# Kernel optimization log

Measured on AMD Instinct MI355X. Metric: run time of the kernel, lower is better.

The kernel has to match this reference:

```python
import jax, jax.numpy as jnp
import numpy as np

MARGIN1 = 0.05
MARGIN2 = 0.09
CAPTION_COUNT = 21
GAMMA = 1.0
P = 0.02
REG = -1.0 / 5.0          # reg passed to ot.sinkhorn (negative, as in the source)
N_ITER = 50               # numItermax=50
B = 8192
N = CAPTION_COUNT + B     # 8213


def _sinkhorn(M):
    """POT ot.sinkhorn (sinkhorn_knopp) with uniform marginals, fixed N_ITER iters.
    K = exp(-M/reg); v = b/(K^T u); u = a/(K v); T = diag(u) K diag(v)."""
    n_a, n_b = M.shape
    K = jnp.exp(-M / REG)                       # note REG < 0 -> exp(5*M)
    a = jnp.full((n_a,), 1.0 / n_a, M.dtype)
    b = jnp.full((n_b,), 1.0 / n_b, M.dtype)
    u0 = jnp.full((n_a,), 1.0 / n_a, M.dtype)
    v0 = jnp.full((n_b,), 1.0 / n_b, M.dtype)

    def body(i, uv):
        u, v = uv
        v = b / (K.T @ u)
        u = a / (K @ v)
        return (u, v)

    u, v = jax.lax.fori_loop(0, N_ITER, body, (u0, v0))
    return u[:, None] * K * v[None, :]


def setup_inputs() -> dict:
    key = jax.random.key(0)
    k1, k2 = jax.random.split(key)
    dist = jax.random.normal(k1, (B, N), dtype=jnp.float32)
    labels = jax.random.randint(k2, (B, N), 0, 4, dtype=jnp.int32)
    return {"dist": dist, "labels": labels}


def reference(dist, labels):
    relu = jax.nn.relu
    # ---- part 1: OT partial-order loss over full dist matrix ----
    scores = dist - dist[:, :1]                                   # subtract column 0
    gm0 = relu(-P - scores) + relu(scores)
    gm1 = relu(MARGIN1 + scores)
    gm2 = relu(-MARGIN2 - scores)
    gm3 = relu(MARGIN2 + scores)
    m0 = (labels == 0).astype(dist.dtype)
    m12 = ((labels == 1) | (labels == 2)).astype(dist.dtype)
    m3 = (labels == 3).astype(dist.dtype)
    GM = m0 * gm0 + m12 * (gm1 + gm2) + m3 * gm3
    expGM = jnp.exp(-GAMMA * GM)
    T = jax.lax.stop_gradient(_sinkhorn(expGM))                   # detached in torch
    T = T / T.sum(axis=1, keepdims=True)
    loss1 = jnp.mean(GM * T)

    # ---- part 2: hinge OT loss on square block dist[:, caption_count:] ----
    s = dist[:, CAPTION_COUNT:]                                   # [B, B]
    s = s - jnp.diagonal(s)[None, :]                              # subtract diag as row
    eye = jnp.eye(s.shape[0], dtype=s.dtype)
    hinge = relu(MARGIN2 + s)
    pos = relu(-0.5 - s)
    GM2 = eye * pos + (1.0 - eye) * hinge
    GM2 = jnp.where(eye > 0.5, 0.0, GM2)                          # masked_fill diag
    expGM2 = jnp.exp(-GAMMA * GM2)
    scores2 = eye * pos + (1.0 - eye) * hinge                     # redefined scores
    T2 = jax.lax.stop_gradient(_sinkhorn(expGM2))
    T2 = jnp.where(eye > 0.5, 0.0, T2)                            # zero diag
    T2 = T2 / T2.sum(axis=1, keepdims=True)
    loss2 = jnp.mean(scores2 * T2)

    return loss1 + loss2
```

## Files before the change

### kernel.cpp

```cpp
#include <hip/hip_runtime.h>

#define R     8192
#define C1    8213
#define C2    8192
#define KROW  8224
#define TROW  8192
#define NKC   514
#define NTC   512
#define CPF   8224

typedef float f32x2 __attribute__((ext_vector_type(2)));

__device__ __forceinline__ void fp8x16_to_f(const int4 w, float f[16]) {
    f32x2 p;
    p = __builtin_amdgcn_cvt_pk_f32_fp8(w.x, false); f[0]  = p.x; f[1]  = p.y;
    p = __builtin_amdgcn_cvt_pk_f32_fp8(w.x, true);  f[2]  = p.x; f[3]  = p.y;
    p = __builtin_amdgcn_cvt_pk_f32_fp8(w.y, false); f[4]  = p.x; f[5]  = p.y;
    p = __builtin_amdgcn_cvt_pk_f32_fp8(w.y, true);  f[6]  = p.x; f[7]  = p.y;
    p = __builtin_amdgcn_cvt_pk_f32_fp8(w.z, false); f[8]  = p.x; f[9]  = p.y;
    p = __builtin_amdgcn_cvt_pk_f32_fp8(w.z, true);  f[10] = p.x; f[11] = p.y;
    p = __builtin_amdgcn_cvt_pk_f32_fp8(w.w, false); f[12] = p.x; f[13] = p.y;
    p = __builtin_amdgcn_cvt_pk_f32_fp8(w.w, true);  f[14] = p.x; f[15] = p.y;
}

__device__ __forceinline__ float fp8_to_f(int byte) {
    f32x2 p = __builtin_amdgcn_cvt_pk_f32_fp8(byte & 0xff, false);
    return p.x;
}

__device__ __forceinline__ float gm_label(float sc, int lab) {
    if (lab == 0) return fmaxf(-0.02f - sc, 0.0f) + fmaxf(sc, 0.0f);
    if (lab == 3) return fmaxf(0.09f + sc, 0.0f);
    return fmaxf(0.05f + sc, 0.0f) + fmaxf(-0.09f - sc, 0.0f);
}

__device__ __forceinline__ float kval(float gm) {
    return __expf(5.0f * __expf(-gm));
}

__device__ __forceinline__ float dotw(const float f[16], float4 w0, float4 w1,
                                      float4 w2, float4 w3, float p) {
    p = fmaf(f[0], w0.x, p);  p = fmaf(f[1], w0.y, p);
    p = fmaf(f[2], w0.z, p);  p = fmaf(f[3], w0.w, p);
    p = fmaf(f[4], w1.x, p);  p = fmaf(f[5], w1.y, p);
    p = fmaf(f[6], w1.z, p);  p = fmaf(f[7], w1.w, p);
    p = fmaf(f[8], w2.x, p);  p = fmaf(f[9], w2.y, p);
    p = fmaf(f[10], w2.z, p); p = fmaf(f[11], w2.w, p);
    p = fmaf(f[12], w3.x, p); p = fmaf(f[13], w3.y, p);
    p = fmaf(f[14], w3.z, p); p = fmaf(f[15], w3.w, p);
    return p;
}


__global__ __launch_bounds__(256) void build_k1(const float* __restrict__ dist,
                                                const int* __restrict__ lab,
                                                unsigned char* __restrict__ K,
                                                unsigned char* __restrict__ gm) {
    int row = blockIdx.y;
    int j0 = (blockIdx.x * 256 + threadIdx.x) * 4;
    if (j0 >= KROW) return;
    size_t ib = (size_t)row * C1;
    float d0 = dist[ib];
    float val[4], gv[4];
#pragma unroll
    for (int k = 0; k < 4; ++k) {
        int j = j0 + k;
        val[k] = 0.0f; gv[k] = 0.0f;
        if (j < C1) {
            float g = gm_label(dist[ib + j] - d0, lab[ib + j]);
            gv[k] = g;
            val[k] = kval(g);
        }
    }
    int p = 0;
    p = __builtin_amdgcn_cvt_pk_fp8_f32(val[0], val[1], p, false);
    p = __builtin_amdgcn_cvt_pk_fp8_f32(val[2], val[3], p, true);
    *reinterpret_cast<int*>(K + (size_t)row * KROW + j0) = p;
    if (gm) {
        int q = 0;
        q = __builtin_amdgcn_cvt_pk_fp8_f32(gv[0], gv[1], q, false);
        q = __builtin_amdgcn_cvt_pk_fp8_f32(gv[2], gv[3], q, true);
        *reinterpret_cast<int*>(gm + (size_t)row * KROW + j0) = q;
    }
}

__global__ __launch_bounds__(256) void diag_k(const float* __restrict__ dist,
                                              float* __restrict__ dcol) {
    int j = blockIdx.x * 256 + threadIdx.x;
    if (j < R) dcol[j] = dist[(size_t)j * C1 + 21 + j];
}

__global__ __launch_bounds__(256) void build_k2(const float* __restrict__ dist,
                                                const float* __restrict__ dcol,
                                                unsigned char* __restrict__ K,
                                                unsigned char* __restrict__ gm) {
    int row = blockIdx.y;
    int j0 = (blockIdx.x * 256 + threadIdx.x) * 4;
    if (j0 >= KROW) return;
    size_t ib = (size_t)row * C1 + 21;
    float val[4], gv[4];
#pragma unroll
    for (int k = 0; k < 4; ++k) {
        int j = j0 + k;
        val[k] = 0.0f; gv[k] = 0.0f;
        if (j < C2) {
            float s = dist[ib + j] - dcol[j];
            float g = (j == row) ? 0.0f : fmaxf(0.09f + s, 0.0f);
            gv[k] = g;
            val[k] = kval(g);
        }
    }
    int p = 0;
    p = __builtin_amdgcn_cvt_pk_fp8_f32(val[0], val[1], p, false);
    p = __builtin_amdgcn_cvt_pk_fp8_f32(val[2], val[3], p, true);
    *reinterpret_cast<int*>(K + (size_t)row * KROW + j0) = p;
    if (gm) {
        int q = 0;
        q = __builtin_amdgcn_cvt_pk_fp8_f32(gv[0], gv[1], q, false);
        q = __builtin_amdgcn_cvt_pk_fp8_f32(gv[2], gv[3], q, true);
        *reinterpret_cast<int*>(gm + (size_t)row * KROW + j0) = q;
    }
}

__global__ __launch_bounds__(256) void transpose_k(const unsigned char* __restrict__ K,
                                                   unsigned char* __restrict__ KT) {
    __shared__ unsigned char tile[64][64];
    int i0 = blockIdx.x * 64;
    int j0 = blockIdx.y * 64;
    int t = threadIdx.x;
    int r = t >> 2, cb = (t & 3) << 4;
    if (j0 + cb < KROW) {
        int4 w = *reinterpret_cast<const int4*>(K + (size_t)(i0 + r) * KROW + j0 + cb);
        *reinterpret_cast<int4*>(&tile[r][cb]) = w;
    }
    __syncthreads();
    int jl = t >> 2, ib = (t & 3) << 4;
    if (j0 + jl < KROW) {
        unsigned char tmp[16];
#pragma unroll
        for (int k = 0; k < 16; ++k) tmp[k] = tile[ib + k][jl];
        *reinterpret_cast<int4*>(KT + (size_t)(j0 + jl) * TROW + i0 + ib) =
            *reinterpret_cast<const int4*>(tmp);
    }
}

__global__ __launch_bounds__(256) void fill_f(float* __restrict__ p, int n, float val) {
    int i = blockIdx.x * 256 + threadIdx.x;
    if (i < n) p[i] = val;
}

__global__ __launch_bounds__(256) void v_pass(const unsigned char* __restrict__ KT,
                                              const float* __restrict__ u,
                                              float* __restrict__ v,
                                              int C, float bval) {
    __shared__ float4 wp[4][516];
    int tx = threadIdx.x;
    {
        const float4* g = reinterpret_cast<const float4*>(u);
        float4 a = g[tx];
        float4 b = g[tx + 256];
        wp[tx & 3][tx >> 2] = a;
        wp[tx & 3][(tx >> 2) + 64] = b;
        float4 c2 = g[tx + 512];
        float4 d2 = g[tx + 768];
        wp[tx & 3][(tx >> 2) + 128] = c2;
        wp[tx & 3][(tx >> 2) + 192] = d2;
        float4 e2 = g[tx + 1024];
        float4 f2 = g[tx + 1280];
        wp[tx & 3][(tx >> 2) + 256] = e2;
        wp[tx & 3][(tx >> 2) + 320] = f2;
        float4 g2 = g[tx + 1536];
        float4 h2 = g[tx + 1792];
        wp[tx & 3][(tx >> 2) + 384] = g2;
        wp[tx & 3][(tx >> 2) + 448] = h2;
    }
    __syncthreads();
    int lane = tx & 63, wv = tx >> 6;
    const int4* KTb = reinterpret_cast<const int4*>(KT);
    int ra = blockIdx.x * 8 + wv * 2;
    const int4* K0 = KTb + (size_t)ra * NTC;
    const int4* K1 = K0 + NTC;
    float p0 = 0.0f, p1 = 0.0f;
#pragma unroll
    for (int s = 0; s < 8; ++s) {
        int ch = s * 64 + lane;
        float4 w0 = wp[0][ch], w1 = wp[1][ch], w2 = wp[2][ch], w3 = wp[3][ch];
        float f[16];
        fp8x16_to_f(K0[ch], f);
        p0 = dotw(f, w0, w1, w2, w3, p0);
        fp8x16_to_f(K1[ch], f);
        p1 = dotw(f, w0, w1, w2, w3, p1);
    }
#pragma unroll
    for (int off = 32; off; off >>= 1) {
        p0 += __shfl_down(p0, off, 64);
        p1 += __shfl_down(p1, off, 64);
    }
    if (lane == 0) {
        v[ra]     = (ra < C)     ? bval / p0 : 0.0f;
        v[ra + 1] = (ra + 1 < C) ? bval / p1 : 0.0f;
    }
}

__global__ __launch_bounds__(256) void u_pass(const unsigned char* __restrict__ K,
                                              const float* __restrict__ v,
                                              float* __restrict__ u, float aval) {
    __shared__ float4 wp[4][516];
    int tx = threadIdx.x;
    {
        const float4* g = reinterpret_cast<const float4*>(v);
#pragma unroll
        for (int k = 0; k < 8; ++k) {
            float4 a = g[tx + k * 256];
            wp[tx & 3][(tx >> 2) + k * 64] = a;
        }
        if (tx < 8) {
            float4 a = g[2048 + tx];
            wp[tx & 3][(tx >> 2) + 512] = a;
        }
    }
    __syncthreads();
    int lane = tx & 63, wv = tx >> 6;
    const int4* Kb = reinterpret_cast<const int4*>(K);
    int ra = blockIdx.x * 8 + wv * 2;
    const int4* K0 = Kb + (size_t)ra * NKC;
    const int4* K1 = K0 + NKC;
    float p0 = 0.0f, p1 = 0.0f;
#pragma unroll
    for (int s = 0; s < 8; ++s) {
        int ch = s * 64 + lane;
        float4 w0 = wp[0][ch], w1 = wp[1][ch], w2 = wp[2][ch], w3 = wp[3][ch];
        float f[16];
        fp8x16_to_f(K0[ch], f);
        p0 = dotw(f, w0, w1, w2, w3, p0);
        fp8x16_to_f(K1[ch], f);
        p1 = dotw(f, w0, w1, w2, w3, p1);
    }
    if (lane < 2) {
        int ch = 512 + lane;
        float4 w0 = wp[0][ch], w1 = wp[1][ch], w2 = wp[2][ch], w3 = wp[3][ch];
        float f[16];
        fp8x16_to_f(K0[ch], f);
        p0 = dotw(f, w0, w1, w2, w3, p0);
        fp8x16_to_f(K1[ch], f);
        p1 = dotw(f, w0, w1, w2, w3, p1);
    }
#pragma unroll
    for (int off = 32; off; off >>= 1) {
        p0 += __shfl_down(p0, off, 64);
        p1 += __shfl_down(p1, off, 64);
    }
    if (lane == 0) {
        u[ra]     = aval / p0;
        u[ra + 1] = aval / p1;
    }
}


__device__ __forceinline__ float2 block_reduce_2(float x, float y, float* sb) {
#pragma unroll
    for (int off = 32; off; off >>= 1) {
        x += __shfl_down(x, off, 64);
        y += __shfl_down(y, off, 64);
    }
    if ((threadIdx.x & 63) == 0) {
        int w = threadIdx.x >> 6;
        sb[w] = x; sb[4 + w] = y;
    }
    __syncthreads();
    float2 r;
    r.x = sb[0] + sb[1] + sb[2] + sb[3];
    r.y = sb[4] + sb[5] + sb[6] + sb[7];
    __syncthreads();
    return r;
}

__global__ __launch_bounds__(256) void loss1_gm(const unsigned char* __restrict__ K,
                                                const unsigned char* __restrict__ GM,
                                                const float* __restrict__ v,
                                                float* __restrict__ ratio) {
    __shared__ float sb[8];
    int i = blockIdx.x;
    const int4* Kr = reinterpret_cast<const int4*>(K + (size_t)i * KROW);
    const int4* Gr = reinterpret_cast<const int4*>(GM + (size_t)i * KROW);
    const float4* v4 = reinterpret_cast<const float4*>(v);
    float num = 0, den = 0;
    for (int c = threadIdx.x; c < NKC; c += 256) {
        float kf[16], gf[16];
        fp8x16_to_f(Kr[c], kf);
        fp8x16_to_f(Gr[c], gf);
#pragma unroll
        for (int q = 0; q < 4; ++q) {
            float4 w = v4[c * 4 + q];
            float k0 = kf[q * 4 + 0] * w.x, k1 = kf[q * 4 + 1] * w.y;
            float k2 = kf[q * 4 + 2] * w.z, k3 = kf[q * 4 + 3] * w.w;
            den += k0 + k1 + k2 + k3;
            num = fmaf(gf[q * 4 + 0], k0, num);
            num = fmaf(gf[q * 4 + 1], k1, num);
            num = fmaf(gf[q * 4 + 2], k2, num);
            num = fmaf(gf[q * 4 + 3], k3, num);
        }
    }
    float2 r = block_reduce_2(num, den, sb);
    if (threadIdx.x == 0) ratio[i] = r.x / r.y;
}

__global__ __launch_bounds__(256) void loss2_gm(const unsigned char* __restrict__ K,
                                                const unsigned char* __restrict__ GM,
                                                const float* __restrict__ v,
                                                float* __restrict__ ratio) {
    __shared__ float sb[8];
    int i = blockIdx.x;
    const int4* Kr = reinterpret_cast<const int4*>(K + (size_t)i * KROW);
    const int4* Gr = reinterpret_cast<const int4*>(GM + (size_t)i * KROW);
    const float4* v4 = reinterpret_cast<const float4*>(v);
    float num = 0, den = 0;
    for (int c = threadIdx.x; c < NKC; c += 256) {
        float kf[16], gf[16];
        fp8x16_to_f(Kr[c], kf);
        fp8x16_to_f(Gr[c], gf);
        int jb = c * 16;
#pragma unroll
        for (int q = 0; q < 4; ++q) {
            float4 w = v4[c * 4 + q];
            float m0 = (jb + q * 4 + 0 == i) ? 0.0f : 1.0f;
            float m1 = (jb + q * 4 + 1 == i) ? 0.0f : 1.0f;
            float m2 = (jb + q * 4 + 2 == i) ? 0.0f : 1.0f;
            float m3 = (jb + q * 4 + 3 == i) ? 0.0f : 1.0f;
            float k0 = kf[q * 4 + 0] * w.x * m0, k1 = kf[q * 4 + 1] * w.y * m1;
            float k2 = kf[q * 4 + 2] * w.z * m2, k3 = kf[q * 4 + 3] * w.w * m3;
            den += k0 + k1 + k2 + k3;
            num = fmaf(gf[q * 4 + 0], k0, num);
            num = fmaf(gf[q * 4 + 1], k1, num);
            num = fmaf(gf[q * 4 + 2], k2, num);
            num = fmaf(gf[q * 4 + 3], k3, num);
        }
    }
    float2 r = block_reduce_2(num, den, sb);
    if (threadIdx.x == 0) ratio[i] = r.x / r.y;
}

__global__ __launch_bounds__(256) void loss1_k(const unsigned char* __restrict__ K,
                                               const float* __restrict__ v,
                                               const float* __restrict__ dist,
                                               const int* __restrict__ lab,
                                               float* __restrict__ ratio) {
    __shared__ float sb[8];
    int i = blockIdx.x;
    size_t ib = (size_t)i * C1;
    float d0 = dist[ib];
    const unsigned char* Kr = K + (size_t)i * KROW;
    float num = 0, den = 0;
    for (int j0 = threadIdx.x * 4; j0 < C1; j0 += 1024) {
        int p = *reinterpret_cast<const int*>(Kr + j0);
#pragma unroll
        for (int k = 0; k < 4; ++k) {
            int j = j0 + k;
            int jc = (j < C1) ? j : (C1 - 1);
            float kv = fp8_to_f(p >> (k * 8)) * v[jc];
            float g = gm_label(dist[ib + jc] - d0, lab[ib + jc]);
            den += kv;
            num = fmaf(g, kv, num);
        }
    }
    float2 r = block_reduce_2(num, den, sb);
    if (threadIdx.x == 0) ratio[i] = r.x / r.y;
}

__global__ __launch_bounds__(256) void loss2_k(const unsigned char* __restrict__ K,
                                               const float* __restrict__ v,
                                               const float* __restrict__ dist,
                                               const float* __restrict__ dcol,
                                               float* __restrict__ ratio) {
    __shared__ float sb[8];
    int i = blockIdx.x;
    const unsigned char* Kr = K + (size_t)i * KROW;
    const float* Dr = dist + (size_t)i * C1 + 21;
    float num = 0, den = 0;
    for (int j0 = threadIdx.x * 4; j0 < C2; j0 += 1024) {
        int p = *reinterpret_cast<const int*>(Kr + j0);
#pragma unroll
        for (int k = 0; k < 4; ++k) {
            int j = j0 + k;
            if (j == i) continue;
            float kv = fp8_to_f(p >> (k * 8)) * v[j];
            float h = fmaxf(0.09f + Dr[j] - dcol[j], 0.0f);
            den += kv;
            num = fmaf(h, kv, num);
        }
    }
    float2 r = block_reduce_2(num, den, sb);
    if (threadIdx.x == 0) ratio[i] = r.x / r.y;
}

__global__ __launch_bounds__(256) void final_k(const float* __restrict__ r1,
                                               const float* __restrict__ r2,
                                               float* __restrict__ out) {
    __shared__ float sb[8];
    float s1 = 0, s2 = 0;
    for (int i = threadIdx.x; i < R; i += 256) { s1 += r1[i]; s2 += r2[i]; }
    float2 t = block_reduce_2(s1, s2, sb);
    if (threadIdx.x == 0)
        out[0] = t.x / ((float)R * (float)C1) + t.y / ((float)R * (float)C2);
}

static void run_phase(const unsigned char* K, const unsigned char* KT,
                      float* u, float* v, int C, hipStream_t stream) {
    float aval = 1.0f / (float)R;
    float bval = 1.0f / (float)C;
    fill_f<<<dim3(R / 256), 256, 0, stream>>>(u, R, aval);
    for (int t = 0; t < 50; ++t) {
        v_pass<<<dim3(CPF / 8), 256, 0, stream>>>(KT, u, v, C, bval);
        if (t < 49)
            u_pass<<<dim3(R / 8), 256, 0, stream>>>(K, v, u, aval);
    }
}

extern "C" void kernel_launch(void* const* d_in, const int* in_sizes, int n_in,
                              void* d_out, int out_size, void* d_ws, size_t ws_size,
                              hipStream_t stream) {
    const float* dist = (const float*)d_in[0];
    const int* lab = (const int*)d_in[1];
    float* out = (float*)d_out;
    char* ws = (char*)d_ws;

    const size_t kbytes = (size_t)R * KROW;
    const size_t tbytes = (size_t)KROW * TROW;
    size_t small = (size_t)CPF * sizeof(float) + 4 * (size_t)R * sizeof(float);
    size_t need_base = kbytes + tbytes + small;
    size_t need_gm = need_base + kbytes;
    if (ws_size < need_base) return;
    bool useGM = ws_size >= need_gm;

    size_t off = 0;
    unsigned char* K = (unsigned char*)(ws + off);  off += kbytes;
    unsigned char* KT = (unsigned char*)(ws + off); off += tbytes;
    unsigned char* GM = nullptr;
    if (useGM) { GM = (unsigned char*)(ws + off); off += kbytes; }
    float* v = (float*)(ws + off);     off += (size_t)CPF * sizeof(float);
    float* u = (float*)(ws + off);     off += (size_t)R * sizeof(float);
    float* dcol = (float*)(ws + off);  off += (size_t)R * sizeof(float);
    float* rat1 = (float*)(ws + off);  off += (size_t)R * sizeof(float);
    float* rat2 = (float*)(ws + off);  off += (size_t)R * sizeof(float);

    int gb = (KROW / 4 + 255) / 256;

    build_k1<<<dim3(gb, R), 256, 0, stream>>>(dist, lab, K, GM);
    transpose_k<<<dim3(R / 64, (KROW + 63) / 64), 256, 0, stream>>>(K, KT);
    run_phase(K, KT, u, v, C1, stream);
    if (useGM)
        loss1_gm<<<dim3(R), 256, 0, stream>>>(K, GM, v, rat1);
    else
        loss1_k<<<dim3(R), 256, 0, stream>>>(K, v, dist, lab, rat1);

    diag_k<<<dim3(R / 256), 256, 0, stream>>>(dist, dcol);
    build_k2<<<dim3(gb, R), 256, 0, stream>>>(dist, dcol, K, GM);
    transpose_k<<<dim3(R / 64, (KROW + 63) / 64), 256, 0, stream>>>(K, KT);
    run_phase(K, KT, u, v, C2, stream);
    if (useGM)
        loss2_gm<<<dim3(R), 256, 0, stream>>>(K, GM, v, rat2);
    else
        loss2_k<<<dim3(R), 256, 0, stream>>>(K, v, dist, dcol, rat2);

    final_k<<<dim3(1), 256, 0, stream>>>(rat1, rat2, out);
}
```

Before: 3.371 ms.

## Run both Sinkhorn problems concurrently in fused dual kernels; stage build loads through LDS

Builds both K matrices (and transposes) up front when the workspace is large enough, then runs the two independent Sinkhorn iterations together in a single v_pass_dual/u_pass_dual launch per half-step. This halves the number of small matvec launches and doubles the grid per launch, so each launch fills the GPU better. The build kernels also switch to aligned float4 loads staged through shared memory instead of unaligned scalar loads. The cost is roughly double the workspace footprint, and the old sequential path is kept as a fallback.

Result: faster. 2.953 ms (-12.4%).

```diff
diff --git a/kernel.cpp b/kernel.cpp
--- a/kernel.cpp
+++ b/kernel.cpp
@@ -8,6 +8,7 @@
 #define NKC   514
 #define NTC   512
 #define CPF   8224
+#define BLKJ  1024
 
 typedef float f32x2 __attribute__((ext_vector_type(2)));
 
@@ -52,14 +53,40 @@
 }
 
 
-__global__ __launch_bounds__(256) void build_k1(const float* __restrict__ dist,
-                                                const int* __restrict__ lab,
-                                                unsigned char* __restrict__ K,
-                                                unsigned char* __restrict__ gm) {
+__global__ __launch_bounds__(256) void build_k1a(const float* __restrict__ dist,
+                                                 const int* __restrict__ lab,
+                                                 unsigned char* __restrict__ K,
+                                                 unsigned char* __restrict__ gm) {
+    __shared__ float ds[BLKJ + 4];
+    __shared__ int dl[BLKJ + 4];
     int row = blockIdx.y;
-    int j0 = (blockIdx.x * 256 + threadIdx.x) * 4;
+    int c0 = blockIdx.x * BLKJ;
+    int tx = threadIdx.x;
+    size_t ib = (size_t)row * C1;
+    int sh = row & 3;
+    long base4 = ((long)ib + c0 - sh) >> 2;
+    const long tot4 = ((long)R * C1) >> 2;
+    {
+        const float4* g4 = reinterpret_cast<const float4*>(dist);
+        const int4* l4 = reinterpret_cast<const int4*>(lab);
+        long i4 = base4 + tx;
+        float4 dv = make_float4(0, 0, 0, 0);
+        int4 lv = make_int4(0, 0, 0, 0);
+        if (i4 >= 0 && i4 < tot4) { dv = g4[i4]; lv = l4[i4]; }
+        *reinterpret_cast<float4*>(&ds[tx * 4]) = dv;
+        *reinterpret_cast<int4*>(&dl[tx * 4]) = lv;
+        if (tx == 0) {
+            long j4 = base4 + 256;
+            float4 dv2 = make_float4(0, 0, 0, 0);
+            int4 lv2 = make_int4(0, 0, 0, 0);
+            if (j4 >= 0 && j4 < tot4) { dv2 = g4[j4]; lv2 = l4[j4]; }
+            *reinterpret_cast<float4*>(&ds[1024]) = dv2;
+            *reinterpret_cast<int4*>(&dl[1024]) = lv2;
+        }
+    }
+    __syncthreads();
+    int j0 = c0 + tx * 4;
     if (j0 >= KROW) return;
-    size_t ib = (size_t)row * C1;
     float d0 = dist[ib];
     float val[4], gv[4];
 #pragma unroll
@@ -67,7 +94,8 @@
         int j = j0 + k;
         val[k] = 0.0f; gv[k] = 0.0f;
         if (j < C1) {
-            float g = gm_label(dist[ib + j] - d0, lab[ib + j]);
+            int li = tx * 4 + sh + k;
+            float g = gm_label(ds[li] - d0, dl[li]);
             gv[k] = g;
             val[k] = kval(g);
         }
@@ -90,21 +118,41 @@
     if (j < R) dcol[j] = dist[(size_t)j * C1 + 21 + j];
 }
 
-__global__ __launch_bounds__(256) void build_k2(const float* __restrict__ dist,
-                                                const float* __restrict__ dcol,
-                                                unsigned char* __restrict__ K,
-                                                unsigned char* __restrict__ gm) {
+__global__ __launch_bounds__(256) void build_k2a(const float* __restrict__ dist,
+                                                 const float* __restrict__ dcol,
+                                                 unsigned char* __restrict__ K,
+                                                 unsigned char* __restrict__ gm) {
+    __shared__ float ds[BLKJ + 4];
     int row = blockIdx.y;
-    int j0 = (blockIdx.x * 256 + threadIdx.x) * 4;
+    int c0 = blockIdx.x * BLKJ;
+    int tx = threadIdx.x;
+    size_t ib = (size_t)row * C1 + 21;
+    int sh = (int)(ib & 3);
+    long base4 = ((long)ib + c0 - sh) >> 2;
+    const long tot4 = ((long)R * C1) >> 2;
+    {
+        const float4* g4 = reinterpret_cast<const float4*>(dist);
+        long i4 = base4 + tx;
+        float4 dv = make_float4(0, 0, 0, 0);
+        if (i4 >= 0 && i4 < tot4) dv = g4[i4];
+        *reinterpret_cast<float4*>(&ds[tx * 4]) = dv;
+        if (tx == 0) {
+            long j4 = base4 + 256;
+            float4 dv2 = make_float4(0, 0, 0, 0);
+            if (j4 >= 0 && j4 < tot4) dv2 = g4[j4];
+            *reinterpret_cast<float4*>(&ds[1024]) = dv2;
+        }
+    }
+    __syncthreads();
+    int j0 = c0 + tx * 4;
     if (j0 >= KROW) return;
-    size_t ib = (size_t)row * C1 + 21;
     float val[4], gv[4];
 #pragma unroll
     for (int k = 0; k < 4; ++k) {
         int j = j0 + k;
         val[k] = 0.0f; gv[k] = 0.0f;
         if (j < C2) {
-            float s = dist[ib + j] - dcol[j];
+            float s = ds[tx * 4 + sh + k] - dcol[j];
             float g = (j == row) ? 0.0f : fmaxf(0.09f + s, 0.0f);
             gv[k] = g;
             val[k] = kval(g);
@@ -149,35 +197,25 @@
     if (i < n) p[i] = val;
 }
 
-__global__ __launch_bounds__(256) void v_pass(const unsigned char* __restrict__ KT,
-                                              const float* __restrict__ u,
-                                              float* __restrict__ v,
-                                              int C, float bval) {
-    __shared__ float4 wp[4][516];
+
+__device__ __forceinline__ void vpass_body(const unsigned char* __restrict__ KT,
+                                           const float* __restrict__ u,
+                                           float* __restrict__ v,
+                                           int bb, int C, float bval,
+                                           float4 (*wp)[516]) {
     int tx = threadIdx.x;
     {
         const float4* g = reinterpret_cast<const float4*>(u);
-        float4 a = g[tx];
-        float4 b = g[tx + 256];
-        wp[tx & 3][tx >> 2] = a;
-        wp[tx & 3][(tx >> 2) + 64] = b;
-        float4 c2 = g[tx + 512];
-        float4 d2 = g[tx + 768];
-        wp[tx & 3][(tx >> 2) + 128] = c2;
-        wp[tx & 3][(tx >> 2) + 192] = d2;
-        float4 e2 = g[tx + 1024];
-        float4 f2 = g[tx + 1280];
-        wp[tx & 3][(tx >> 2) + 256] = e2;
-        wp[tx & 3][(tx >> 2) + 320] = f2;
-        float4 g2 = g[tx + 1536];
-        float4 h2 = g[tx + 1792];
-        wp[tx & 3][(tx >> 2) + 384] = g2;
-        wp[tx & 3][(tx >> 2) + 448] = h2;
+#pragma unroll
+        for (int k = 0; k < 8; ++k) {
+            float4 a = g[tx + k * 256];
+            wp[tx & 3][(tx >> 2) + k * 64] = a;
+        }
     }
     __syncthreads();
     int lane = tx & 63, wv = tx >> 6;
     const int4* KTb = reinterpret_cast<const int4*>(KT);
-    int ra = blockIdx.x * 8 + wv * 2;
+    int ra = bb * 8 + wv * 2;
     const int4* K0 = KTb + (size_t)ra * NTC;
     const int4* K1 = K0 + NTC;
     float p0 = 0.0f, p1 = 0.0f;
@@ -202,10 +240,11 @@
     }
 }
 
-__global__ __launch_bounds__(256) void u_pass(const unsigned char* __restrict__ K,
-                                              const float* __restrict__ v,
-                                              float* __restrict__ u, float aval) {
-    __shared__ float4 wp[4][516];
+__device__ __forceinline__ void upass_body(const unsigned char* __restrict__ K,
+                                           const float* __restrict__ v,
+                                           float* __restrict__ u,
+                                           int bb, float aval,
+                                           float4 (*wp)[516]) {
     int tx = threadIdx.x;
     {
         const float4* g = reinterpret_cast<const float4*>(v);
@@ -222,7 +261,7 @@
     __syncthreads();
     int lane = tx & 63, wv = tx >> 6;
     const int4* Kb = reinterpret_cast<const int4*>(K);
-    int ra = blockIdx.x * 8 + wv * 2;
+    int ra = bb * 8 + wv * 2;
     const int4* K0 = Kb + (size_t)ra * NKC;
     const int4* K1 = K0 + NKC;
     float p0 = 0.0f, p1 = 0.0f;
@@ -254,6 +293,45 @@
         u[ra]     = aval / p0;
         u[ra + 1] = aval / p1;
     }
+}
+
+__global__ __launch_bounds__(256) void v_pass(const unsigned char* __restrict__ KT,
+                                              const float* __restrict__ u,
+                                              float* __restrict__ v, int C, float bval) {
+    __shared__ float4 wp[4][516];
+    vpass_body(KT, u, v, blockIdx.x, C, bval, wp);
+}
+
+__global__ __launch_bounds__(256) void u_pass(const unsigned char* __restrict__ K,
+                                              const float* __restrict__ v,
+                                              float* __restrict__ u, float aval) {
+    __shared__ float4 wp[4][516];
+    upass_body(K, v, u, blockIdx.x, aval, wp);
+}
+
+__global__ __launch_bounds__(256) void v_pass_dual(const unsigned char* __restrict__ KT1,
+                                                   const unsigned char* __restrict__ KT2,
+                                                   const float* __restrict__ u,
+                                                   float* __restrict__ v,
+                                                   float bval1, float bval2) {
+    __shared__ float4 wp[4][516];
+    int b = blockIdx.x;
+    if (b < 1028)
+        vpass_body(KT1, u, v, b, C1, bval1, wp);
+    else
+        vpass_body(KT2, u + R, v + CPF, b - 1028, C2, bval2, wp);
+}
+
+__global__ __launch_bounds__(256) void u_pass_dual(const unsigned char* __restrict__ K1,
+                                                   const unsigned char* __restrict__ K2,
+                                                   const float* __restrict__ v,
+                                                   float* __restrict__ u, float aval) {
+    __shared__ float4 wp[4][516];
+    int b = blockIdx.x;
+    if (b < 1024)
+        upass_body(K1, v, u, b, aval, wp);
+    else
+        upass_body(K2, v + CPF, u + R, b - 1024, aval, wp);
 }
 
 
@@ -404,8 +482,8 @@
         out[0] = t.x / ((float)R * (float)C1) + t.y / ((float)R * (float)C2);
 }
 
-static void run_phase(const unsigned char* K, const unsigned char* KT,
-                      float* u, float* v, int C, hipStream_t stream) {
+static void run_phase_seq(const unsigned char* K, const unsigned char* KT,
+                          float* u, float* v, int C, hipStream_t stream) {
     float aval = 1.0f / (float)R;
     float bval = 1.0f / (float)C;
     fill_f<<<dim3(R / 256), 256, 0, stream>>>(u, R, aval);
@@ -424,39 +502,74 @@
     float* out = (float*)d_out;
     char* ws = (char*)d_ws;
 
-    const size_t kbytes = (size_t)R * KROW;
-    const size_t tbytes = (size_t)KROW * TROW;
-    size_t small = (size_t)CPF * sizeof(float) + 4 * (size_t)R * sizeof(float);
-    size_t need_base = kbytes + tbytes + small;
-    size_t need_gm = need_base + kbytes;
+    const size_t kb = (size_t)R * KROW;
+    const size_t small_dual = (2 * (size_t)CPF + 2 * R + 3 * R) * sizeof(float);
+    const size_t small_seq = ((size_t)CPF + 4 * R) * sizeof(float);
+    const size_t need_dual = 6 * kb + small_dual;
+    const size_t need_gm_seq = 3 * kb + small_seq;
+    const size_t need_base = 2 * kb + small_seq;
     if (ws_size < need_base) return;
-    bool useGM = ws_size >= need_gm;
-
+
+    const float aval = 1.0f / (float)R;
+    const int gbx = (KROW + BLKJ - 1) / BLKJ;
+    const dim3 gT(R / 64, (KROW + 63) / 64);
+
+    if (ws_size >= need_dual) {
+        size_t off = 0;
+        unsigned char* K1 = (unsigned char*)(ws + off);  off += kb;
+        unsigned char* K2 = (unsigned char*)(ws + off);  off += kb;
+        unsigned char* K1T = (unsigned char*)(ws + off); off += kb;
+        unsigned char* K2T = (unsigned char*)(ws + off); off += kb;
+        unsigned char* GM1 = (unsigned char*)(ws + off); off += kb;
+        unsigned char* GM2 = (unsigned char*)(ws + off); off += kb;
+        float* v = (float*)(ws + off);    off += 2 * (size_t)CPF * sizeof(float);
+        float* u = (float*)(ws + off);    off += 2 * (size_t)R * sizeof(float);
+        float* dcol = (float*)(ws + off); off += (size_t)R * sizeof(float);
+        float* rat1 = (float*)(ws + off); off += (size_t)R * sizeof(float);
+        float* rat2 = (float*)(ws + off); off += (size_t)R * sizeof(float);
+
+        diag_k<<<dim3(R / 256), 256, 0, stream>>>(dist, dcol);
+        build_k1a<<<dim3(gbx, R), 256, 0, stream>>>(dist, lab, K1, GM1);
+        build_k2a<<<dim3(gbx, R), 256, 0, stream>>>(dist, dcol, K2, GM2);
+        transpose_k<<<gT, 256, 0, stream>>>(K1, K1T);
+        transpose_k<<<gT, 256, 0, stream>>>(K2, K2T);
+        fill_f<<<dim3(2 * R / 256), 256, 0, stream>>>(u, 2 * R, aval);
+        for (int t = 0; t < 50; ++t) {
+            v_pass_dual<<<dim3(2 * (CPF / 8)), 256, 0, stream>>>(
+                K1T, K2T, u, v, 1.0f / (float)C1, 1.0f / (float)C2);
+            if (t < 49)
+                u_pass_dual<<<dim3(2 * (R / 8)), 256, 0, stream>>>(K1, K2, v, u, aval);
+        }
+        loss1_gm<<<dim3(R), 256, 0, stream>>>(K1, GM1, v, rat1);
+        loss2_gm<<<dim3(R), 256, 0, stream>>>(K2, GM2, v + CPF, rat2);
+        final_k<<<dim3(1), 256, 0, stream>>>(rat1, rat2, out);
+        return;
+    }
+
+    bool useGM = ws_size >= need_gm_seq;
     size_t off = 0;
-    unsigned char* K = (unsigned char*)(ws + off);  off += kbytes;
-    unsigned char* KT = (unsigned char*)(ws + off); off += tbytes;
+    unsigned char* K = (unsigned char*)(ws + off);  off += kb;
+    unsigned char* KT = (unsigned char*)(ws + off); off += kb;
     unsigned char* GM = nullptr;
-    if (useGM) { GM = (unsigned char*)(ws + off); off += kbytes; }
-    float* v = (float*)(ws + off);     off += (size_t)CPF * sizeof(float);
-    float* u = (float*)(ws + off);     off += (size_t)R * sizeof(float);
-    float* dcol = (float*)(ws + off);  off += (size_t)R * sizeof(float);
-    float* rat1 = (float*)(ws + off);  off += (size_t)R * sizeof(float);
-    float* rat2 = (float*)(ws + off);  off += (size_t)R * sizeof(float);
-
-    int gb = (KROW / 4 + 255) / 256;
-
-    build_k1<<<dim3(gb, R), 256, 0, stream>>>(dist, lab, K, GM);
-    transpose_k<<<dim3(R / 64, (KROW + 63) / 64), 256, 0, stream>>>(K, KT);
-    run_phase(K, KT, u, v, C1, stream);
+    if (useGM) { GM = (unsigned char*)(ws + off); off += kb; }
+    float* v = (float*)(ws + off);    off += (size_t)CPF * sizeof(float);
+    float* u = (float*)(ws + off);    off += (size_t)R * sizeof(float);
+    float* dcol = (float*)(ws + off); off += (size_t)R * sizeof(float);
+    float* rat1 = (float*)(ws + off); off += (size_t)R * sizeof(float);
+    float* rat2 = (float*)(ws + off); off += (size_t)R * sizeof(float);
+
+    build_k1a<<<dim3(gbx, R), 256, 0, stream>>>(dist, lab, K, GM);
+    transpose_k<<<gT, 256, 0, stream>>>(K, KT);
+    run_phase_seq(K, KT, u, v, C1, stream);
     if (useGM)
         loss1_gm<<<dim3(R), 256, 0, stream>>>(K, GM, v, rat1);
     else
         loss1_k<<<dim3(R), 256, 0, stream>>>(K, v, dist, lab, rat1);
 
     diag_k<<<dim3(R / 256), 256, 0, stream>>>(dist, dcol);
-    build_k2<<<dim3(gb, R), 256, 0, stream>>>(dist, dcol, K, GM);
-    transpose_k<<<dim3(R / 64, (KROW + 63) / 64), 256, 0, stream>>>(K, KT);
-    run_phase(K, KT, u, v, C2, stream);
+    build_k2a<<<dim3(gbx, R), 256, 0, stream>>>(dist, dcol, K, GM);
+    transpose_k<<<gT, 256, 0, stream>>>(K, KT);
+    run_phase_seq(K, KT, u, v, C2, stream);
     if (useGM)
         loss2_gm<<<dim3(R), 256, 0, stream>>>(K, GM, v, rat2);
     else
```
